# Optimization experiments

Measured on AMD Instinct MI355X. Metric: run time of the kernel, lower is better.

The kernel has to match this reference:

```python
import jax, jax.numpy as jnp
import numpy as np

N_USER = 100000
N_ITEM = 100000
IN_DIM = 256
H = 128
EPS = 1e-5


def _segment_mean(x, idx, num_segments):
    s = jax.ops.segment_sum(x, idx, num_segments=num_segments)
    c = jax.ops.segment_sum(jnp.ones((idx.shape[0], 1), x.dtype), idx, num_segments=num_segments)
    return s / jnp.maximum(c, 1.0)


def _sage(x_src, x_dst, ei, wl, bl, wr):
    # PyG SAGEConv(mean): lin_l(mean_j x_src[j]) + lin_r(x_dst); lin_r has no bias
    agg = _segment_mean(x_src[ei[0]], ei[1], x_dst.shape[0])  # [N_dst, H]
    return agg @ wl.T + bl + x_dst @ wr.T


def _ln(x, g, b):
    mu = jnp.mean(x, axis=-1, keepdims=True)
    var = jnp.mean(jnp.square(x - mu), axis=-1, keepdims=True)
    return (x - mu) * jax.lax.rsqrt(var + EPS) * g + b


def setup_inputs() -> dict:
    key = jax.random.key(0)
    ks = jax.random.split(key, 32)
    d = {
        "x_user": jax.random.normal(ks[0], (N_USER, IN_DIM), jnp.float32),
        "x_item": jax.random.normal(ks[1], (N_ITEM, IN_DIM), jnp.float32),
        "ei_rates": jax.random.randint(ks[2], (2, 600000), 0, N_USER, jnp.int32),
        "ei_rev": jax.random.randint(ks[3], (2, 600000), 0, N_ITEM, jnp.int32),
        "proj_user_w": jax.random.normal(ks[4], (H, IN_DIM), jnp.float32) * 0.05,
        "proj_user_b": jnp.zeros((H,), jnp.float32),
        "proj_item_w": jax.random.normal(ks[5], (H, IN_DIM), jnp.float32) * 0.05,
        "proj_item_b": jnp.zeros((H,), jnp.float32),
        "ln_user_g": jnp.ones((H,), jnp.float32),
        "ln_user_b": jnp.zeros((H,), jnp.float32),
        "ln_item_g": jnp.ones((H,), jnp.float32),
        "ln_item_b": jnp.zeros((H,), jnp.float32),
    }
    i = 6
    for l in range(2):
        for rel in ("rates", "rev"):
            d[f"l{l}_{rel}_wl"] = jax.random.normal(ks[i], (H, H), jnp.float32) * 0.05; i += 1
            d[f"l{l}_{rel}_bl"] = jnp.zeros((H,), jnp.float32)
            d[f"l{l}_{rel}_wr"] = jax.random.normal(ks[i], (H, H), jnp.float32) * 0.05; i += 1
    return d


def reference(x_user, x_item, ei_rates, ei_rev,
              proj_user_w, proj_user_b, proj_item_w, proj_item_b,
              ln_user_g, ln_user_b, ln_item_g, ln_item_b,
              l0_rates_wl, l0_rates_bl, l0_rates_wr,
              l0_rev_wl, l0_rev_bl, l0_rev_wr,
              l1_rates_wl, l1_rates_bl, l1_rates_wr,
              l1_rev_wl, l1_rev_bl, l1_rev_wr):
    # input projection: Linear -> ReLU (dropout is identity in eval / p=0)
    hu = jax.nn.relu(x_user @ proj_user_w.T + proj_user_b)  # [N_user, H]
    hi = jax.nn.relu(x_item @ proj_item_w.T + proj_item_b)  # [N_item, H]
    layers = [
        (l0_rates_wl, l0_rates_bl, l0_rates_wr, l0_rev_wl, l0_rev_bl, l0_rev_wr),
        (l1_rates_wl, l1_rates_bl, l1_rates_wr, l1_rev_wl, l1_rev_bl, l1_rev_wr),
    ]
    for li, (rwl, rbl, rwr, vwl, vbl, vwr) in enumerate(layers):
        # relation user--rates-->item and item--rev_rates-->user
        out_item = _sage(hu, hi, ei_rates, rwl, rbl, rwr)
        out_user = _sage(hi, hu, ei_rev, vwl, vbl, vwr)
        hu = _ln(hu + out_user, ln_user_g, ln_user_b)
        hi = _ln(hi + out_item, ln_item_g, ln_item_b)
        if li < len(layers) - 1:
            hu = jax.nn.relu(hu)
            hi = jax.nn.relu(hi)
    return jnp.stack([hu, hi])  # [2, 100000, 128]
```

## Files before the change

kernel.cpp:

```cpp
#include <hip/hip_runtime.h>

#define H 128
#define IN_DIM 256
#define NNODE 100000
#define NEDGE 600000
#define LN_EPS 1e-5f
#define CAP 32
#define LDSK 264

typedef float f32x4 __attribute__((ext_vector_type(4)));
typedef short bf16x8 __attribute__((ext_vector_type(8)));
typedef short s16x4 __attribute__((ext_vector_type(4)));

__device__ __forceinline__ short f2bf(float f) {
    unsigned u = __float_as_uint(f);
    return (short)((u + 0x7fff + ((u >> 16) & 1)) >> 16);
}
__device__ __forceinline__ float bf2f(short h) {
    return __uint_as_float(((unsigned)(unsigned short)h) << 16);
}
__device__ __forceinline__ float grp16_sum(float v) {
    v += __shfl_xor(v, 1);
    v += __shfl_xor(v, 2);
    v += __shfl_xor(v, 4);
    v += __shfl_xor(v, 8);
    return v;
}

__global__ __launch_bounds__(256) void fill_bucket_kernel(
    const int* __restrict__ ei, int* __restrict__ deg, int* __restrict__ bucket,
    int E) {
    const int e = blockIdx.x * blockDim.x + threadIdx.x;
    if (e >= E) return;
    const int src = ei[e];
    const int dst = ei[E + e];
    const int pos = atomicAdd(deg + dst, 1);
    if (pos < CAP) bucket[(size_t)dst * CAP + pos] = src;
}

__global__ __launch_bounds__(512) void agg_mean_kernel(
    const float* __restrict__ hsrc, const int* __restrict__ bucket,
    const int* __restrict__ deg, float* __restrict__ agg, int M) {
    const int lane = threadIdx.x & 63;
    const int wid = __builtin_amdgcn_readfirstlane(
        blockIdx.x * (blockDim.x >> 6) + (threadIdx.x >> 6));
    const int nw = gridDim.x * (blockDim.x >> 6);
    const int c2 = lane * 2;

    for (int d = wid; d < M; d += nw) {
        const int n = __builtin_amdgcn_readfirstlane(deg[d]);
        const int nn = n < CAP ? n : CAP;
        const int* bk = bucket + (size_t)d * CAP;
        float2 acc = make_float2(0.f, 0.f);
        int j = 0;
        for (; j + 4 <= nn; j += 4) {
            const int4 s4 = *(const int4*)(bk + j);
            const float2 v0 = *(const float2*)(hsrc + (size_t)s4.x * H + c2);
            const float2 v1 = *(const float2*)(hsrc + (size_t)s4.y * H + c2);
            const float2 v2 = *(const float2*)(hsrc + (size_t)s4.z * H + c2);
            const float2 v3 = *(const float2*)(hsrc + (size_t)s4.w * H + c2);
            acc.x += (v0.x + v1.x) + (v2.x + v3.x);
            acc.y += (v0.y + v1.y) + (v2.y + v3.y);
        }
        for (; j < nn; j++) {
            const int s = bk[j];
            const float2 v = *(const float2*)(hsrc + (size_t)s * H + c2);
            acc.x += v.x;
            acc.y += v.y;
        }
        const float inv = 1.0f / fmaxf((float)n, 1.0f);
        *(float2*)(agg + (size_t)d * H + c2) =
            make_float2(acc.x * inv, acc.y * inv);
    }
}

template <int MODE>
__global__ __launch_bounds__(512, 2) void gemm_fused_kernel(
    const float* __restrict__ A0, const float* __restrict__ A1,
    const float* __restrict__ W0, const float* __restrict__ W1,
    const float* __restrict__ bias, const float* __restrict__ g,
    const float* __restrict__ b, float* __restrict__ out, int M, int do_relu) {
    __shared__ short Whi[128 * LDSK];
    __shared__ short Wlo[128 * LDSK];

    for (int base = threadIdx.x * 4; base < 128 * 256; base += 512 * 4) {
        const int n = base >> 8;
        const int k = base & 255;
        float4 w;
        if (MODE == 0) {
            w = *(const float4*)(W0 + n * 256 + k);
        } else {
            w = (k < 128) ? *(const float4*)(W0 + n * 128 + k)
                          : *(const float4*)(W1 + n * 128 + (k - 128));
        }
        const float wf[4] = {w.x, w.y, w.z, w.w};
        s16x4 hi, lo;
#pragma unroll
        for (int i = 0; i < 4; i++) {
            const short h = f2bf(wf[i]);
            hi[i] = h;
            lo[i] = f2bf(wf[i] - bf2f(h));
        }
        *(s16x4*)&Whi[n * LDSK + k] = hi;
        *(s16x4*)&Wlo[n * LDSK + k] = lo;
    }
    __syncthreads();

    const int lane = threadIdx.x & 63;
    const int wave = threadIdx.x >> 6;
    const int q = lane >> 4;
    const int cl = lane & 15;
    const int mrow0 = blockIdx.x * 256 + wave * 32;

    f32x4 acc[2][8];
#pragma unroll
    for (int mr = 0; mr < 2; mr++)
#pragma unroll
        for (int nr = 0; nr < 8; nr++) acc[mr][nr] = (f32x4)0.f;

    const int bbase = cl * LDSK + q * 8;

#pragma unroll
    for (int ks = 0; ks < 8; ks++) {
        const float* Asrc;
        int kk;
        if (MODE == 0) {
            Asrc = A0;
            kk = ks * 32;
        } else if (ks < 4) {
            Asrc = A0;
            kk = ks * 32;
        } else {
            Asrc = A1;
            kk = ks * 32 - 128;
        }
        const int strideA = (MODE == 0) ? IN_DIM : H;

        bf16x8 ahi[2], alo[2];
#pragma unroll
        for (int mr = 0; mr < 2; mr++) {
            int m = mrow0 + mr * 16 + cl;
            if (m >= M) m = M - 1;
            const float* p = Asrc + (size_t)m * strideA + kk + q * 8;
            const float4 x0 = *(const float4*)p;
            const float4 x1 = *(const float4*)(p + 4);
            const float xf[8] = {x0.x, x0.y, x0.z, x0.w,
                                 x1.x, x1.y, x1.z, x1.w};
#pragma unroll
            for (int i = 0; i < 8; i++) {
                const short h = f2bf(xf[i]);
                ahi[mr][i] = h;
                alo[mr][i] = f2bf(xf[i] - bf2f(h));
            }
        }

#pragma unroll
        for (int nr = 0; nr < 8; nr++) {
            const int boff = bbase + nr * 16 * LDSK + ks * 32;
            const bf16x8 bhi = *(const bf16x8*)&Whi[boff];
            const bf16x8 blo = *(const bf16x8*)&Wlo[boff];
            acc[0][nr] = __builtin_amdgcn_mfma_f32_16x16x32_bf16(
                ahi[0], bhi, acc[0][nr], 0, 0, 0);
            acc[1][nr] = __builtin_amdgcn_mfma_f32_16x16x32_bf16(
                ahi[1], bhi, acc[1][nr], 0, 0, 0);
            acc[0][nr] = __builtin_amdgcn_mfma_f32_16x16x32_bf16(
                ahi[0], blo, acc[0][nr], 0, 0, 0);
            acc[1][nr] = __builtin_amdgcn_mfma_f32_16x16x32_bf16(
                ahi[1], blo, acc[1][nr], 0, 0, 0);
            acc[0][nr] = __builtin_amdgcn_mfma_f32_16x16x32_bf16(
                alo[0], bhi, acc[0][nr], 0, 0, 0);
            acc[1][nr] = __builtin_amdgcn_mfma_f32_16x16x32_bf16(
                alo[1], bhi, acc[1][nr], 0, 0, 0);
        }
    }

    float blv[8], gv[8], bv[8];
#pragma unroll
    for (int nr = 0; nr < 8; nr++) {
        const int col = nr * 16 + cl;
        blv[nr] = bias[col];
        if (MODE == 1) {
            gv[nr] = g[col];
            bv[nr] = b[col];
        }
    }

#pragma unroll
    for (int mr = 0; mr < 2; mr++) {
#pragma unroll
        for (int reg = 0; reg < 4; reg++) {
            const int m = mrow0 + mr * 16 + q * 4 + reg;
            if (MODE == 0) {
                if (m < M) {
#pragma unroll
                    for (int nr = 0; nr < 8; nr++)
                        out[(size_t)m * H + nr * 16 + cl] =
                            fmaxf(acc[mr][nr][reg] + blv[nr], 0.f);
                }
            } else {
                float h[8];
                float s = 0.f;
#pragma unroll
                for (int nr = 0; nr < 8; nr++) {
                    const float xr =
                        (m < M) ? A1[(size_t)m * H + nr * 16 + cl] : 0.f;
                    h[nr] = xr + acc[mr][nr][reg] + blv[nr];
                    s += h[nr];
                }
                const float mu = grp16_sum(s) * (1.0f / 128.0f);
                float v = 0.f;
#pragma unroll
                for (int nr = 0; nr < 8; nr++) {
                    const float d = h[nr] - mu;
                    v += d * d;
                }
                const float var = grp16_sum(v) * (1.0f / 128.0f);
                const float rs = 1.0f / sqrtf(var + LN_EPS);
                if (m < M) {
#pragma unroll
                    for (int nr = 0; nr < 8; nr++) {
                        float o = (h[nr] - mu) * rs * gv[nr] + bv[nr];
                        if (do_relu) o = fmaxf(o, 0.f);
                        out[(size_t)m * H + nr * 16 + cl] = o;
                    }
                }
            }
        }
    }
}

extern "C" void kernel_launch(void* const* d_in, const int* in_sizes, int n_in,
                              void* d_out, int out_size, void* d_ws,
                              size_t ws_size, hipStream_t stream) {
    const float* x_user = (const float*)d_in[0];
    const float* x_item = (const float*)d_in[1];
    const int* ei_rates = (const int*)d_in[2];
    const int* ei_rev = (const int*)d_in[3];
    const float* proj_user_w = (const float*)d_in[4];
    const float* proj_user_b = (const float*)d_in[5];
    const float* proj_item_w = (const float*)d_in[6];
    const float* proj_item_b = (const float*)d_in[7];
    const float* ln_user_g = (const float*)d_in[8];
    const float* ln_user_b = (const float*)d_in[9];
    const float* ln_item_g = (const float*)d_in[10];
    const float* ln_item_b = (const float*)d_in[11];
    const float* lw[2][2][3];
    {
        int idx = 12;
        for (int l = 0; l < 2; l++)
            for (int rel = 0; rel < 2; rel++)
                for (int p = 0; p < 3; p++)
                    lw[l][rel][p] = (const float*)d_in[idx++];
    }

    const size_t NH = (size_t)NNODE * H;
    float* ws = (float*)d_ws;
    float* agg_u = ws;
    float* agg_i = ws + NH;
    int* deg_i = (int*)(ws + 2 * NH);
    int* deg_u = deg_i + NNODE;
    int* bkt_i = deg_u + NNODE;
    int* bkt_u = bkt_i + (size_t)NNODE * CAP;

    float* hu = (float*)d_out;
    float* hi = (float*)d_out + NH;

    const int NGB = (NNODE + 255) / 256;

    hipMemsetAsync(deg_i, 0, 2 * NNODE * sizeof(int), stream);
    fill_bucket_kernel<<<(NEDGE + 255) / 256, 256, 0, stream>>>(ei_rates, deg_i,
                                                                bkt_i, NEDGE);
    fill_bucket_kernel<<<(NEDGE + 255) / 256, 256, 0, stream>>>(ei_rev, deg_u,
                                                                bkt_u, NEDGE);

    gemm_fused_kernel<0><<<NGB, 512, 0, stream>>>(
        x_user, nullptr, proj_user_w, nullptr, proj_user_b, nullptr, nullptr,
        hu, NNODE, 0);
    gemm_fused_kernel<0><<<NGB, 512, 0, stream>>>(
        x_item, nullptr, proj_item_w, nullptr, proj_item_b, nullptr, nullptr,
        hi, NNODE, 0);

    for (int l = 0; l < 2; l++) {
        agg_mean_kernel<<<2048, 512, 0, stream>>>(hu, bkt_i, deg_i, agg_i,
                                                  NNODE);
        agg_mean_kernel<<<2048, 512, 0, stream>>>(hi, bkt_u, deg_u, agg_u,
                                                  NNODE);

        const int relu = (l == 0) ? 1 : 0;
        gemm_fused_kernel<1><<<NGB, 512, 0, stream>>>(
            agg_i, hi, lw[l][0][0], lw[l][0][2], lw[l][0][1], ln_item_g,
            ln_item_b, hi, NNODE, relu);
        gemm_fused_kernel<1><<<NGB, 512, 0, stream>>>(
            agg_u, hu, lw[l][1][0], lw[l][1][2], lw[l][1][1], ln_user_g,
            ln_user_b, hu, NNODE, relu);
    }
}
```

Before: 846.3 us.

## Store hidden states as split bf16 and merge user/item launches

```diff
diff --git a/kernel.cpp b/kernel.cpp
--- a/kernel.cpp
+++ b/kernel.cpp
@@ -6,7 +6,7 @@
 #define NEDGE 600000
 #define LN_EPS 1e-5f
 #define CAP 32
-#define LDSK 264
+#define LDSK2 136
 
 typedef float f32x4 __attribute__((ext_vector_type(4)));
 typedef short bf16x8 __attribute__((ext_vector_type(8)));
@@ -18,6 +18,11 @@
 }
 __device__ __forceinline__ float bf2f(short h) {
     return __uint_as_float(((unsigned)(unsigned short)h) << 16);
+}
+__device__ __forceinline__ unsigned packbf(float f) {
+    const short hi = f2bf(f);
+    const short lo = f2bf(f - bf2f(hi));
+    return (((unsigned)(unsigned short)hi) << 16) | (unsigned)(unsigned short)lo;
 }
 __device__ __forceinline__ float grp16_sum(float v) {
     v += __shfl_xor(v, 1);
@@ -39,78 +44,85 @@
 }
 
 __global__ __launch_bounds__(512) void agg_mean_kernel(
-    const float* __restrict__ hsrc, const int* __restrict__ bucket,
-    const int* __restrict__ deg, float* __restrict__ agg, int M) {
+    const ushort* __restrict__ huHi, const ushort* __restrict__ hiHi,
+    const int* __restrict__ bktI, const int* __restrict__ degI,
+    const int* __restrict__ bktU, const int* __restrict__ degU,
+    unsigned* __restrict__ aggI, unsigned* __restrict__ aggU) {
     const int lane = threadIdx.x & 63;
     const int wid = __builtin_amdgcn_readfirstlane(
         blockIdx.x * (blockDim.x >> 6) + (threadIdx.x >> 6));
     const int nw = gridDim.x * (blockDim.x >> 6);
     const int c2 = lane * 2;
 
-    for (int d = wid; d < M; d += nw) {
-        const int n = __builtin_amdgcn_readfirstlane(deg[d]);
+    for (int t = wid; t < 2 * NNODE; t += nw) {
+        const int isU = (t >= NNODE);
+        const int d = isU ? t - NNODE : t;
+        const ushort* src = isU ? hiHi : huHi;
+        const int* bk = (isU ? bktU : bktI) + (size_t)d * CAP;
+        const int n = __builtin_amdgcn_readfirstlane((isU ? degU : degI)[d]);
         const int nn = n < CAP ? n : CAP;
-        const int* bk = bucket + (size_t)d * CAP;
-        float2 acc = make_float2(0.f, 0.f);
+        unsigned* dst = (isU ? aggU : aggI) + (size_t)d * H;
+
+        float ax = 0.f, ay = 0.f;
         int j = 0;
         for (; j + 4 <= nn; j += 4) {
             const int4 s4 = *(const int4*)(bk + j);
-            const float2 v0 = *(const float2*)(hsrc + (size_t)s4.x * H + c2);
-            const float2 v1 = *(const float2*)(hsrc + (size_t)s4.y * H + c2);
-            const float2 v2 = *(const float2*)(hsrc + (size_t)s4.z * H + c2);
-            const float2 v3 = *(const float2*)(hsrc + (size_t)s4.w * H + c2);
-            acc.x += (v0.x + v1.x) + (v2.x + v3.x);
-            acc.y += (v0.y + v1.y) + (v2.y + v3.y);
+            const unsigned v0 = *(const unsigned*)(src + (size_t)s4.x * H + c2);
+            const unsigned v1 = *(const unsigned*)(src + (size_t)s4.y * H + c2);
+            const unsigned v2 = *(const unsigned*)(src + (size_t)s4.z * H + c2);
+            const unsigned v3 = *(const unsigned*)(src + (size_t)s4.w * H + c2);
+            ax += bf2f((short)(v0 & 0xffff)) + bf2f((short)(v1 & 0xffff)) +
+                  bf2f((short)(v2 & 0xffff)) + bf2f((short)(v3 & 0xffff));
+            ay += bf2f((short)(v0 >> 16)) + bf2f((short)(v1 >> 16)) +
+                  bf2f((short)(v2 >> 16)) + bf2f((short)(v3 >> 16));
         }
         for (; j < nn; j++) {
-            const int s = bk[j];
-            const float2 v = *(const float2*)(hsrc + (size_t)s * H + c2);
-            acc.x += v.x;
-            acc.y += v.y;
+            const unsigned v =
+                *(const unsigned*)(src + (size_t)bk[j] * H + c2);
+            ax += bf2f((short)(v & 0xffff));
+            ay += bf2f((short)(v >> 16));
         }
         const float inv = 1.0f / fmaxf((float)n, 1.0f);
-        *(float2*)(agg + (size_t)d * H + c2) =
-            make_float2(acc.x * inv, acc.y * inv);
-    }
-}
-
-template <int MODE>
-__global__ __launch_bounds__(512, 2) void gemm_fused_kernel(
-    const float* __restrict__ A0, const float* __restrict__ A1,
-    const float* __restrict__ W0, const float* __restrict__ W1,
-    const float* __restrict__ bias, const float* __restrict__ g,
-    const float* __restrict__ b, float* __restrict__ out, int M, int do_relu) {
-    __shared__ short Whi[128 * LDSK];
-    __shared__ short Wlo[128 * LDSK];
-
-    for (int base = threadIdx.x * 4; base < 128 * 256; base += 512 * 4) {
-        const int n = base >> 8;
-        const int k = base & 255;
-        float4 w;
-        if (MODE == 0) {
-            w = *(const float4*)(W0 + n * 256 + k);
-        } else {
-            w = (k < 128) ? *(const float4*)(W0 + n * 128 + k)
-                          : *(const float4*)(W1 + n * 128 + (k - 128));
-        }
-        const float wf[4] = {w.x, w.y, w.z, w.w};
-        s16x4 hi, lo;
-#pragma unroll
-        for (int i = 0; i < 4; i++) {
-            const short h = f2bf(wf[i]);
-            hi[i] = h;
-            lo[i] = f2bf(wf[i] - bf2f(h));
-        }
-        *(s16x4*)&Whi[n * LDSK + k] = hi;
-        *(s16x4*)&Wlo[n * LDSK + k] = lo;
-    }
-    __syncthreads();
+        uint2 w;
+        w.x = packbf(ax * inv);
+        w.y = packbf(ay * inv);
+        *(uint2*)(dst + c2) = w;
+    }
+}
+
+template <int MODE, int OUTF>
+__global__ __launch_bounds__(512, 4) void gemm_fused(
+    const float* __restrict__ xA, const float* __restrict__ xB,
+    const unsigned* __restrict__ pkA, const unsigned* __restrict__ pkB,
+    const ushort* __restrict__ hAhi, const ushort* __restrict__ hAlo,
+    const ushort* __restrict__ hBhi, const ushort* __restrict__ hBlo,
+    const float* __restrict__ wA0, const float* __restrict__ wA1,
+    const float* __restrict__ wB0, const float* __restrict__ wB1,
+    const float* __restrict__ biasA, const float* __restrict__ biasB,
+    const float* __restrict__ gA, const float* __restrict__ bA,
+    const float* __restrict__ gB, const float* __restrict__ bB,
+    ushort* __restrict__ oAhi, ushort* __restrict__ oAlo,
+    ushort* __restrict__ oBhi, ushort* __restrict__ oBlo,
+    float* __restrict__ foA, float* __restrict__ foB, int M, int NT,
+    int relu) {
+    __shared__ short Whi[H * LDSK2];
+    __shared__ short Wlo[H * LDSK2];
+
+    const int sel = (blockIdx.x >= NT);
+    const int tile = blockIdx.x - (sel ? NT : 0);
+    const float* W0 = sel ? wB0 : wA0;
+    const float* W1 = sel ? wB1 : wA1;
+    const unsigned* Apk = sel ? pkB : pkA;
+    const ushort* Hhi = sel ? hBhi : hAhi;
+    const ushort* Hlo = sel ? hBlo : hAlo;
+    const float* xI = sel ? xB : xA;
+    const float* bias = sel ? biasB : biasA;
 
     const int lane = threadIdx.x & 63;
     const int wave = threadIdx.x >> 6;
     const int q = lane >> 4;
     const int cl = lane & 15;
-    const int mrow0 = blockIdx.x * 256 + wave * 32;
+    const int mrow0 = tile * 256 + wave * 32;
 
     f32x4 acc[2][8];
 #pragma unroll
@@ -118,61 +130,96 @@
 #pragma unroll
         for (int nr = 0; nr < 8; nr++) acc[mr][nr] = (f32x4)0.f;
 
-    const int bbase = cl * LDSK + q * 8;
-
-#pragma unroll
-    for (int ks = 0; ks < 8; ks++) {
-        const float* Asrc;
-        int kk;
-        if (MODE == 0) {
-            Asrc = A0;
-            kk = ks * 32;
-        } else if (ks < 4) {
-            Asrc = A0;
-            kk = ks * 32;
-        } else {
-            Asrc = A1;
-            kk = ks * 32 - 128;
-        }
-        const int strideA = (MODE == 0) ? IN_DIM : H;
-
-        bf16x8 ahi[2], alo[2];
-#pragma unroll
-        for (int mr = 0; mr < 2; mr++) {
-            int m = mrow0 + mr * 16 + cl;
-            if (m >= M) m = M - 1;
-            const float* p = Asrc + (size_t)m * strideA + kk + q * 8;
-            const float4 x0 = *(const float4*)p;
-            const float4 x1 = *(const float4*)(p + 4);
-            const float xf[8] = {x0.x, x0.y, x0.z, x0.w,
-                                 x1.x, x1.y, x1.z, x1.w};
-#pragma unroll
-            for (int i = 0; i < 8; i++) {
-                const short h = f2bf(xf[i]);
-                ahi[mr][i] = h;
-                alo[mr][i] = f2bf(xf[i] - bf2f(h));
+#pragma unroll
+    for (int p = 0; p < 2; p++) {
+        if (p) __syncthreads();
+        for (int i = threadIdx.x * 4; i < H * 128; i += 512 * 4) {
+            const int n = i >> 7;
+            const int k = i & 127;
+            float4 w;
+            if (MODE == 0)
+                w = *(const float4*)(W0 + n * IN_DIM + p * 128 + k);
+            else
+                w = *(const float4*)((p ? W1 : W0) + n * H + k);
+            const float wf[4] = {w.x, w.y, w.z, w.w};
+            s16x4 hi, lo;
+#pragma unroll
+            for (int i2 = 0; i2 < 4; i2++) {
+                const short h = f2bf(wf[i2]);
+                hi[i2] = h;
+                lo[i2] = f2bf(wf[i2] - bf2f(h));
             }
-        }
-
-#pragma unroll
-        for (int nr = 0; nr < 8; nr++) {
-            const int boff = bbase + nr * 16 * LDSK + ks * 32;
-            const bf16x8 bhi = *(const bf16x8*)&Whi[boff];
-            const bf16x8 blo = *(const bf16x8*)&Wlo[boff];
-            acc[0][nr] = __builtin_amdgcn_mfma_f32_16x16x32_bf16(
-                ahi[0], bhi, acc[0][nr], 0, 0, 0);
-            acc[1][nr] = __builtin_amdgcn_mfma_f32_16x16x32_bf16(
-                ahi[1], bhi, acc[1][nr], 0, 0, 0);
-            acc[0][nr] = __builtin_amdgcn_mfma_f32_16x16x32_bf16(
-                ahi[0], blo, acc[0][nr], 0, 0, 0);
-            acc[1][nr] = __builtin_amdgcn_mfma_f32_16x16x32_bf16(
-                ahi[1], blo, acc[1][nr], 0, 0, 0);
-            acc[0][nr] = __builtin_amdgcn_mfma_f32_16x16x32_bf16(
-                alo[0], bhi, acc[0][nr], 0, 0, 0);
-            acc[1][nr] = __builtin_amdgcn_mfma_f32_16x16x32_bf16(
-                alo[1], bhi, acc[1][nr], 0, 0, 0);
-        }
-    }
+            *(s16x4*)&Whi[n * LDSK2 + k] = hi;
+            *(s16x4*)&Wlo[n * LDSK2 + k] = lo;
+        }
+        __syncthreads();
+
+#pragma unroll
+        for (int ks2 = 0; ks2 < 4; ks2++) {
+            bf16x8 ahi[2], alo[2];
+#pragma unroll
+            for (int mr = 0; mr < 2; mr++) {
+                int m = mrow0 + mr * 16 + cl;
+                if (m >= M) m = M - 1;
+                const int koff = ks2 * 32 + q * 8;
+                if (MODE == 0) {
+                    const float* ptr =
+                        xI + (size_t)m * IN_DIM + p * 128 + koff;
+                    const float4 x0 = *(const float4*)ptr;
+                    const float4 x1 = *(const float4*)(ptr + 4);
+                    const float xf[8] = {x0.x, x0.y, x0.z, x0.w,
+                                         x1.x, x1.y, x1.z, x1.w};
+#pragma unroll
+                    for (int i = 0; i < 8; i++) {
+                        const short h = f2bf(xf[i]);
+                        ahi[mr][i] = h;
+                        alo[mr][i] = f2bf(xf[i] - bf2f(h));
+                    }
+                } else if (p == 0) {
+                    const unsigned* ptr = Apk + (size_t)m * H + koff;
+                    const uint4 v0 = *(const uint4*)ptr;
+                    const uint4 v1 = *(const uint4*)(ptr + 4);
+                    const unsigned vf[8] = {v0.x, v0.y, v0.z, v0.w,
+                                            v1.x, v1.y, v1.z, v1.w};
+#pragma unroll
+                    for (int i = 0; i < 8; i++) {
+                        ahi[mr][i] = (short)(vf[i] >> 16);
+                        alo[mr][i] = (short)(vf[i] & 0xffff);
+                    }
+                } else {
+                    const ushort* ph = Hhi + (size_t)m * H + koff;
+                    const ushort* pl = Hlo + (size_t)m * H + koff;
+                    ahi[mr] = *(const bf16x8*)ph;
+                    alo[mr] = *(const bf16x8*)pl;
+                }
+            }
+#pragma unroll
+            for (int nr = 0; nr < 8; nr++) {
+                const int boff =
+                    cl * LDSK2 + q * 8 + nr * 16 * LDSK2 + ks2 * 32;
+                const bf16x8 bhi = *(const bf16x8*)&Whi[boff];
+                const bf16x8 blo = *(const bf16x8*)&Wlo[boff];
+                acc[0][nr] = __builtin_amdgcn_mfma_f32_16x16x32_bf16(
+                    ahi[0], bhi, acc[0][nr], 0, 0, 0);
+                acc[1][nr] = __builtin_amdgcn_mfma_f32_16x16x32_bf16(
+                    ahi[1], bhi, acc[1][nr], 0, 0, 0);
+                acc[0][nr] = __builtin_amdgcn_mfma_f32_16x16x32_bf16(
+                    ahi[0], blo, acc[0][nr], 0, 0, 0);
+                acc[1][nr] = __builtin_amdgcn_mfma_f32_16x16x32_bf16(
+                    ahi[1], blo, acc[1][nr], 0, 0, 0);
+                acc[0][nr] = __builtin_amdgcn_mfma_f32_16x16x32_bf16(
+                    alo[0], bhi, acc[0][nr], 0, 0, 0);
+                acc[1][nr] = __builtin_amdgcn_mfma_f32_16x16x32_bf16(
+                    alo[1], bhi, acc[1][nr], 0, 0, 0);
+            }
+        }
+    }
+
+    ushort* Ohi = sel ? oBhi : oAhi;
+    ushort* Olo = sel ? oBlo : oAlo;
+    float* FO = sel ? foB : foA;
+    const float* gp = sel ? gB : gA;
+    const float* bp = sel ? bB : bA;
 
     float blv[8], gv[8], bv[8];
 #pragma unroll
@@ -180,8 +227,8 @@
         const int col = nr * 16 + cl;
         blv[nr] = bias[col];
         if (MODE == 1) {
-            gv[nr] = g[col];
-            bv[nr] = b[col];
+            gv[nr] = gp[col];
+            bv[nr] = bp[col];
         }
     }
 
@@ -190,20 +237,27 @@
 #pragma unroll
         for (int reg = 0; reg < 4; reg++) {
             const int m = mrow0 + mr * 16 + q * 4 + reg;
+            const bool ok = (m < M);
             if (MODE == 0) {
-                if (m < M) {
-#pragma unroll
-                    for (int nr = 0; nr < 8; nr++)
-                        out[(size_t)m * H + nr * 16 + cl] =
-                            fmaxf(acc[mr][nr][reg] + blv[nr], 0.f);
+                if (ok) {
+#pragma unroll
+                    for (int nr = 0; nr < 8; nr++) {
+                        const float o = fmaxf(acc[mr][nr][reg] + blv[nr], 0.f);
+                        const short hi = f2bf(o);
+                        const size_t off = (size_t)m * H + nr * 16 + cl;
+                        Ohi[off] = (ushort)hi;
+                        Olo[off] = (ushort)f2bf(o - bf2f(hi));
+                    }
                 }
             } else {
                 float h[8];
                 float s = 0.f;
 #pragma unroll
                 for (int nr = 0; nr < 8; nr++) {
+                    const size_t off = (size_t)m * H + nr * 16 + cl;
                     const float xr =
-                        (m < M) ? A1[(size_t)m * H + nr * 16 + cl] : 0.f;
+                        ok ? bf2f((short)Hhi[off]) + bf2f((short)Hlo[off])
+                           : 0.f;
                     h[nr] = xr + acc[mr][nr][reg] + blv[nr];
                     s += h[nr];
                 }
@@ -216,12 +270,19 @@
                 }
                 const float var = grp16_sum(v) * (1.0f / 128.0f);
                 const float rs = 1.0f / sqrtf(var + LN_EPS);
-                if (m < M) {
+                if (ok) {
 #pragma unroll
                     for (int nr = 0; nr < 8; nr++) {
                         float o = (h[nr] - mu) * rs * gv[nr] + bv[nr];
-                        if (do_relu) o = fmaxf(o, 0.f);
-                        out[(size_t)m * H + nr * 16 + cl] = o;
+                        if (relu) o = fmaxf(o, 0.f);
+                        const size_t off = (size_t)m * H + nr * 16 + cl;
+                        if (OUTF) {
+                            FO[off] = o;
+                        } else {
+                            const short hi = f2bf(o);
+                            Ohi[off] = (ushort)hi;
+                            Olo[off] = (ushort)f2bf(o - bf2f(hi));
+                        }
                     }
                 }
             }
@@ -254,44 +315,53 @@
     }
 
     const size_t NH = (size_t)NNODE * H;
-    float* ws = (float*)d_ws;
-    float* agg_u = ws;
-    float* agg_i = ws + NH;
-    int* deg_i = (int*)(ws + 2 * NH);
-    int* deg_u = deg_i + NNODE;
-    int* bkt_i = deg_u + NNODE;
-    int* bkt_u = bkt_i + (size_t)NNODE * CAP;
-
-    float* hu = (float*)d_out;
-    float* hi = (float*)d_out + NH;
-
-    const int NGB = (NNODE + 255) / 256;
-
-    hipMemsetAsync(deg_i, 0, 2 * NNODE * sizeof(int), stream);
-    fill_bucket_kernel<<<(NEDGE + 255) / 256, 256, 0, stream>>>(ei_rates, deg_i,
-                                                                bkt_i, NEDGE);
-    fill_bucket_kernel<<<(NEDGE + 255) / 256, 256, 0, stream>>>(ei_rev, deg_u,
-                                                                bkt_u, NEDGE);
-
-    gemm_fused_kernel<0><<<NGB, 512, 0, stream>>>(
-        x_user, nullptr, proj_user_w, nullptr, proj_user_b, nullptr, nullptr,
-        hu, NNODE, 0);
-    gemm_fused_kernel<0><<<NGB, 512, 0, stream>>>(
-        x_item, nullptr, proj_item_w, nullptr, proj_item_b, nullptr, nullptr,
-        hi, NNODE, 0);
+    ushort* base = (ushort*)d_ws;
+    ushort* huHi = base;
+    ushort* huLo = base + NH;
+    ushort* hiHi = base + 2 * NH;
+    ushort* hiLo = base + 3 * NH;
+    int* degI = (int*)(base + 4 * NH);
+    int* degU = degI + NNODE;
+    int* bktI = degU + NNODE;
+    int* bktU = bktI + (size_t)NNODE * CAP;
+
+    unsigned* aggU = (unsigned*)d_out;
+    unsigned* aggI = aggU + NH;
+    float* foU = (float*)d_out;
+    float* foI = foU + NH;
+
+    const int NT = (NNODE + 255) / 256;
+
+    hipMemsetAsync(degI, 0, 2 * NNODE * sizeof(int), stream);
+    fill_bucket_kernel<<<(NEDGE + 255) / 256, 256, 0, stream>>>(ei_rates, degI,
+                                                                bktI, NEDGE);
+    fill_bucket_kernel<<<(NEDGE + 255) / 256, 256, 0, stream>>>(ei_rev, degU,
+                                                                bktU, NEDGE);
+
+    gemm_fused<0, 0><<<2 * NT, 512, 0, stream>>>(
+        x_user, x_item, nullptr, nullptr, nullptr, nullptr, nullptr, nullptr,
+        proj_user_w, nullptr, proj_item_w, nullptr, proj_user_b, proj_item_b,
+        nullptr, nullptr, nullptr, nullptr, huHi, huLo, hiHi, hiLo, nullptr,
+        nullptr, NNODE, NT, 1);
 
     for (int l = 0; l < 2; l++) {
-        agg_mean_kernel<<<2048, 512, 0, stream>>>(hu, bkt_i, deg_i, agg_i,
-                                                  NNODE);
-        agg_mean_kernel<<<2048, 512, 0, stream>>>(hi, bkt_u, deg_u, agg_u,
-                                                  NNODE);
-
+        agg_mean_kernel<<<2048, 512, 0, stream>>>(huHi, hiHi, bktI, degI,
+                                                  bktU, degU, aggI, aggU);
         const int relu = (l == 0) ? 1 : 0;
-        gemm_fused_kernel<1><<<NGB, 512, 0, stream>>>(
-            agg_i, hi, lw[l][0][0], lw[l][0][2], lw[l][0][1], ln_item_g,
-            ln_item_b, hi, NNODE, relu);
-        gemm_fused_kernel<1><<<NGB, 512, 0, stream>>>(
-            agg_u, hu, lw[l][1][0], lw[l][1][2], lw[l][1][1], ln_user_g,
-            ln_user_b, hu, NNODE, relu);
-    }
-}
+        if (l == 0) {
+            gemm_fused<1, 0><<<2 * NT, 512, 0, stream>>>(
+                nullptr, nullptr, aggU, aggI, huHi, huLo, hiHi, hiLo,
+                lw[0][1][0], lw[0][1][2], lw[0][0][0], lw[0][0][2],
+                lw[0][1][1], lw[0][0][1], ln_user_g, ln_user_b, ln_item_g,
+                ln_item_b, huHi, huLo, hiHi, hiLo, nullptr, nullptr, NNODE,
+                NT, relu);
+        } else {
+            gemm_fused<1, 1><<<2 * NT, 512, 0, stream>>>(
+                nullptr, nullptr, aggU, aggI, huHi, huLo, hiHi, hiLo,
+                lw[1][1][0], lw[1][1][2], lw[1][0][0], lw[1][0][2],
+                lw[1][1][1], lw[1][0][1], ln_user_g, ln_user_b, ln_item_g,
+                ln_item_b, nullptr, nullptr, nullptr, nullptr, foU, foI,
+                NNODE, NT, relu);
+        }
+    }
+}
```

New measurement: 771.2 us. 8.9% less time.
